# Performance work log

Hardware: AMD Instinct MI355X
Metric: run time of the kernel (lower is better)

The kernel has to match this reference:

```python
import jax, jax.numpy as jnp
import numpy as np

B, C, H, W = 4, 512, 64, 64
CQ = C // 8


def setup_inputs() -> dict:
    key = jax.random.key(0)
    k1, k2, k3, k4, k5 = jax.random.split(key, 5)
    return {
        "x": jax.random.normal(k1, (B, C, H, W), dtype=jnp.float32),
        "Wq": jax.random.normal(k2, (CQ, C), dtype=jnp.float32) * (2.0 / C) ** 0.5,
        "Wk": jax.random.normal(k3, (CQ, C), dtype=jnp.float32) * (2.0 / C) ** 0.5,
        "Wv": jax.random.normal(k4, (C, C), dtype=jnp.float32) * (2.0 / C) ** 0.5,
        "gamma": jax.random.normal(k5, (1,), dtype=jnp.float32),
    }


def reference(x, Wq, Wk, Wv, gamma):
    b, c, h, w = x.shape
    n = h * w
    xf = x.reshape(b, c, n)                       # (B, C, N)
    # 1x1 convs (bias=False, norm=identity) == channel matmuls
    q = jnp.einsum('qc,bcn->bnq', Wq, xf)         # (B, N, Cq) -- proj_query permuted
    k = jnp.einsum('qc,bcm->bqm', Wk, xf)         # (B, Cq, N) -- proj_key
    energy = jnp.einsum('bnq,bqm->bnm', q, k)     # (B, N, N)
    attn = jax.nn.softmax(energy, axis=-1)        # softmax over keys (last dim)
    v = jnp.einsum('dc,bcm->bdm', Wv, xf)         # (B, C, N) -- proj_value
    # out = bmm(V, attn^T): out[b,d,n] = sum_m V[b,d,m] * attn[b,n,m]
    out = jnp.einsum('bdm,bnm->bdn', v, attn).reshape(b, c, h, w)
    return gamma * out + x
```

## Files before the change

kernel.cpp:

```cpp
#include <hip/hip_runtime.h>

#define B_  4
#define C_  512
#define CQ_ 64
#define N_  4096
#define LOG2E 1.44269504088896f

typedef _Float16 half8 __attribute__((ext_vector_type(8)));
typedef _Float16 half4 __attribute__((ext_vector_type(4)));
typedef float    f32x4 __attribute__((ext_vector_type(4)));

__device__ __forceinline__ void g2l16(const void* g, void* l) {
  __builtin_amdgcn_global_load_lds(
      (const __attribute__((address_space(1))) void*)g,
      (__attribute__((address_space(3))) void*)l, 16, 0, 0);
}

__global__ __launch_bounds__(256) void wcvt_kernel(
    const float* __restrict__ Wq, const float* __restrict__ Wk,
    const float* __restrict__ Wv, _Float16* __restrict__ Wh)
{
  const int row = blockIdx.x;
  const float* src;
  float s = 1.0f;
  if (row < 64)       { src = Wq + (size_t)row * C_; s = LOG2E; }
  else if (row < 128) { src = Wk + (size_t)(row - 64) * C_; }
  else                { src = Wv + (size_t)(row - 128) * C_; }
  for (int c = threadIdx.x; c < C_; c += 256)
    Wh[(size_t)row * C_ + c] = (_Float16)(src[c] * s);
}

__global__ __launch_bounds__(256) void proj_kernel(
    const float* __restrict__ x, const _Float16* __restrict__ Wh,
    _Float16* __restrict__ Qh, _Float16* __restrict__ Kh, _Float16* __restrict__ Vh)
{
  __shared__ _Float16 xs[32][520];

  const int tid = threadIdx.x;
  const int wid = tid >> 6, lane = tid & 63, ln = lane & 15, lh = lane >> 4;

  const int wg = (blockIdx.x & 7) * 64 + (blockIdx.x >> 3);
  const int b  = wg >> 7;
  const int n0 = (wg & 127) * 32;

  {
    const int nn = (tid & 7) * 4;
    const int c0 = tid >> 3;
    #pragma unroll 4
    for (int cc = 0; cc < 16; ++cc) {
      const int c = cc * 32 + c0;
      f32x4 v = *(const f32x4*)&x[((size_t)b * C_ + c) * N_ + n0 + nn];
      #pragma unroll
      for (int u = 0; u < 4; ++u) xs[nn + u][c] = (_Float16)v[u];
    }
  }
  __syncthreads();

  for (int chT = 0; chT < 10; ++chT) {
    f32x4 acc[2] = {};
    const _Float16* wrow = Wh + (size_t)(chT * 64 + wid * 16 + ln) * C_;

    #pragma unroll 4
    for (int kt = 0; kt < C_; kt += 32) {
      half8 a = *(const half8*)&wrow[kt + lh * 8];
      #pragma unroll
      for (int ct = 0; ct < 2; ++ct) {
        half8 bf = *(const half8*)&xs[ct * 16 + ln][kt + lh * 8];
        acc[ct] = __builtin_amdgcn_mfma_f32_16x16x32_f16(a, bf, acc[ct], 0, 0, 0);
      }
    }

    #pragma unroll
    for (int ct = 0; ct < 2; ++ct) {
      const int n = n0 + ct * 16 + ln;
      #pragma unroll
      for (int j = 0; j < 4; ++j) {
        const int chL = wid * 16 + lh * 4 + j;
        const _Float16 v = (_Float16)acc[ct][j];
        if (chT == 0)      Qh[((size_t)b * N_ + n) * CQ_ + chL] = v;
        else if (chT == 1) Kh[((size_t)b * N_ + n) * CQ_ + chL] = v;
        else               Vh[((size_t)b * C_ + (chT - 2) * 64 + chL) * N_ + n] = v;
      }
    }
  }
}

__global__ __launch_bounds__(512, 2) void stats_kernel(
    const _Float16* __restrict__ Qh, const _Float16* __restrict__ Kh,
    float* __restrict__ m_g, float* __restrict__ il_g)
{
  __shared__ float Ms[8][64];
  __shared__ float Ss[8][64];

  const int tid = threadIdx.x;
  const int wid = tid >> 6, lane = tid & 63, ln = lane & 15, lh = lane >> 4;
  const int b  = blockIdx.x >> 6;
  const int qb = (blockIdx.x & 63) * 64;

  half8 qf[4][2];
  #pragma unroll
  for (int rt = 0; rt < 4; ++rt)
    #pragma unroll
    for (int h = 0; h < 2; ++h)
      qf[rt][h] = *(const half8*)&Qh[((size_t)b * N_ + qb + rt * 16 + ln) * CQ_ + h * 32 + lh * 8];

  float mx[4] = {-3.0e38f, -3.0e38f, -3.0e38f, -3.0e38f};
  float sm[4] = {0.f, 0.f, 0.f, 0.f};

  const _Float16* kp = Kh + ((size_t)b * N_ + wid * 16 + ln) * CQ_ + lh * 8;

  for (int it = 0; it < 32; ++it) {
    const _Float16* kq = kp + (size_t)(it * 128) * CQ_;
    half8 k0 = *(const half8*)kq;
    half8 k1 = *(const half8*)(kq + 32);
    #pragma unroll
    for (int rt = 0; rt < 4; ++rt) {
      f32x4 e = {};
      e = __builtin_amdgcn_mfma_f32_16x16x32_f16(k0, qf[rt][0], e, 0, 0, 0);
      e = __builtin_amdgcn_mfma_f32_16x16x32_f16(k1, qf[rt][1], e, 0, 0, 0);
      const float m1 = fmaxf(fmaxf(e[0], e[1]), fmaxf(e[2], e[3]));
      const float mn = fmaxf(mx[rt], m1);
      sm[rt] = sm[rt] * exp2f(mx[rt] - mn)
             + exp2f(e[0] - mn) + exp2f(e[1] - mn)
             + exp2f(e[2] - mn) + exp2f(e[3] - mn);
      mx[rt] = mn;
    }
  }

  #pragma unroll
  for (int rt = 0; rt < 4; ++rt) {
    float m = mx[rt], s = sm[rt];
    #pragma unroll
    for (int mask = 16; mask <= 32; mask <<= 1) {
      const float om = __shfl_xor(m, mask);
      const float os = __shfl_xor(s, mask);
      const float mn = fmaxf(m, om);
      s = s * exp2f(m - mn) + os * exp2f(om - mn);
      m = mn;
    }
    if (lane < 16) { Ms[wid][rt * 16 + lane] = m; Ss[wid][rt * 16 + lane] = s; }
  }
  __syncthreads();
  if (tid < 64) {
    float m = Ms[0][tid], s = Ss[0][tid];
    #pragma unroll
    for (int w = 1; w < 8; ++w) {
      const float om = Ms[w][tid], os = Ss[w][tid];
      const float mn = fmaxf(m, om);
      s = s * exp2f(m - mn) + os * exp2f(om - mn);
      m = mn;
    }
    m_g[(size_t)b * N_ + qb + tid]  = m;
    il_g[(size_t)b * N_ + qb + tid] = 1.0f / s;
  }
}

__global__ __launch_bounds__(256) void pwrite_kernel(
    const _Float16* __restrict__ Qh, const _Float16* __restrict__ Kh,
    const float* __restrict__ m_g, const float* __restrict__ il_g,
    _Float16* __restrict__ P, int b0)
{
  __shared__ _Float16 Pl[64 * 260];

  const int tid = threadIdx.x;
  const int wid = tid >> 6, lane = tid & 63, ln = lane & 15, lh = lane >> 4;
  const int mb = blockIdx.x * 256;
  const int qb = blockIdx.y * 64;
  const int bz = blockIdx.z;
  const int b  = b0 + bz;

  float m_l[4], il_l[4];
  #pragma unroll
  for (int rt = 0; rt < 4; ++rt) {
    m_l[rt]  = m_g [(size_t)b * N_ + qb + rt * 16 + ln];
    il_l[rt] = il_g[(size_t)b * N_ + qb + rt * 16 + ln];
  }

  half8 qf[4][2];
  #pragma unroll
  for (int rt = 0; rt < 4; ++rt)
    #pragma unroll
    for (int h = 0; h < 2; ++h)
      qf[rt][h] = *(const half8*)&Qh[((size_t)b * N_ + qb + rt * 16 + ln) * CQ_ + h * 32 + lh * 8];

  half8 kf[4][2];
  #pragma unroll
  for (int ms = 0; ms < 4; ++ms)
    #pragma unroll
    for (int h = 0; h < 2; ++h)
      kf[ms][h] = *(const half8*)&Kh[((size_t)b * N_ + mb + wid * 64 + ms * 16 + ln) * CQ_ + h * 32 + lh * 8];

  #pragma unroll
  for (int ms = 0; ms < 4; ++ms) {
    #pragma unroll
    for (int rt = 0; rt < 4; ++rt) {
      f32x4 e = {};
      e = __builtin_amdgcn_mfma_f32_16x16x32_f16(kf[ms][0], qf[rt][0], e, 0, 0, 0);
      e = __builtin_amdgcn_mfma_f32_16x16x32_f16(kf[ms][1], qf[rt][1], e, 0, 0, 0);
      half4 pv;
      #pragma unroll
      for (int j = 0; j < 4; ++j)
        pv[j] = (_Float16)(exp2f(e[j] - m_l[rt]) * il_l[rt]);
      *(half4*)&Pl[(rt * 16 + ln) * 260 + wid * 64 + ms * 16 + lh * 4] = pv;
    }
  }
  __syncthreads();

  const int row = tid >> 2;
  const int cb  = (tid & 3) * 8;
  #pragma unroll
  for (int i = 0; i < 8; ++i) {
    half8 v = *(const half8*)&Pl[row * 260 + cb + i * 32];
    *(half8*)&P[((size_t)bz * N_ + qb + row) * N_ + mb + cb + i * 32] = v;
  }
}

__global__ __launch_bounds__(512) void pv_kernel(
    const float* __restrict__ x, const _Float16* __restrict__ Vh,
    const _Float16* __restrict__ P, const float* __restrict__ gamma,
    float* __restrict__ out, int b0, int nwg)
{
  __shared__ _Float16 As[3][256 * 64];
  __shared__ _Float16 Bs[3][128 * 64];

  const int tid = threadIdx.x;
  const int wid = tid >> 6, lane = tid & 63, ln = lane & 15, lh = lane >> 4;

  const int q8 = nwg >> 3;
  const int wg = (blockIdx.x & 7) * q8 + (blockIdx.x >> 3);
  const int dt = wg & 1;
  const int nt = (wg >> 1) & 31;
  const int bz = wg >> 6;
  const int b  = b0 + bz;
  const int d0 = dt * 256, n0 = nt * 128;

  const _Float16* Ab = Vh + ((size_t)b * C_ + d0) * N_;
  const _Float16* Bb = P  + ((size_t)bz * N_ + n0) * N_;

  const int srow   = lane >> 3;
  const int schunk = lane & 7;
  const _Float16* aSrc[4];
  const _Float16* bSrc[2];
  #pragma unroll
  for (int r = 0; r < 4; ++r) {
    const int row = r * 64 + wid * 8 + srow;
    aSrc[r] = Ab + (size_t)row * N_ + ((schunk ^ (row & 7)) << 3);
  }
  #pragma unroll
  for (int r = 0; r < 2; ++r) {
    const int row = r * 64 + wid * 8 + srow;
    bSrc[r] = Bb + (size_t)row * N_ + ((schunk ^ (row & 7)) << 3);
  }

  auto stage = [&](int buf, int t) {
    const int m0 = t << 6;
    #pragma unroll
    for (int r = 0; r < 4; ++r)
      g2l16(aSrc[r] + m0, (char*)&As[buf][0] + r * 8192 + wid * 1024);
    #pragma unroll
    for (int r = 0; r < 2; ++r)
      g2l16(bSrc[r] + m0, (char*)&Bs[buf][0] + r * 8192 + wid * 1024);
  };

  const int wr = wid >> 1, wc = wid & 1;
  f32x4 acc[4][4] = {};
  const int swl = ln & 7;

  stage(0, 0);
  stage(1, 1);

  for (int t = 0; t < 64; ++t) {
    if (t < 63) { asm volatile("s_waitcnt vmcnt(6)" ::: "memory"); }
    else        { asm volatile("s_waitcnt vmcnt(0)" ::: "memory"); }
    __builtin_amdgcn_s_barrier();
    __builtin_amdgcn_sched_barrier(0);

    const int buf = t % 3;
    const _Float16* Ar = &As[buf][0];
    const _Float16* Br = &Bs[buf][0];

    half8 a[4][2], bq[4][2];
    #pragma unroll
    for (int ft = 0; ft < 4; ++ft) {
      const int row = wr * 64 + ft * 16 + ln;
      #pragma unroll
      for (int kk = 0; kk < 2; ++kk)
        a[ft][kk] = *(const half8*)&Ar[row * 64 + ((((kk << 2) | lh) ^ swl) << 3)];
    }
    #pragma unroll
    for (int gt = 0; gt < 4; ++gt) {
      const int row = wc * 64 + gt * 16 + ln;
      #pragma unroll
      for (int kk = 0; kk < 2; ++kk)
        bq[gt][kk] = *(const half8*)&Br[row * 64 + ((((kk << 2) | lh) ^ swl) << 3)];
    }

    if (t < 62) stage((t + 2) % 3, t + 2);

    #pragma unroll
    for (int kk = 0; kk < 2; ++kk)
      #pragma unroll
      for (int ft = 0; ft < 4; ++ft)
        #pragma unroll
        for (int gt = 0; gt < 4; ++gt)
          acc[ft][gt] = __builtin_amdgcn_mfma_f32_16x16x32_f16(a[ft][kk], bq[gt][kk], acc[ft][gt], 0, 0, 0);
  }

  const float g = gamma[0];
  #pragma unroll
  for (int ft = 0; ft < 4; ++ft) {
    #pragma unroll
    for (int gt = 0; gt < 4; ++gt) {
      #pragma unroll
      for (int j = 0; j < 4; ++j) {
        const int d = d0 + wr * 64 + ft * 16 + lh * 4 + j;
        const int n = n0 + wc * 64 + gt * 16 + ln;
        const size_t idx = ((size_t)b * C_ + d) * N_ + n;
        out[idx] = g * acc[ft][gt][j] + x[idx];
      }
    }
  }
}

extern "C" void kernel_launch(void* const* d_in, const int* in_sizes, int n_in,
                              void* d_out, int out_size, void* d_ws, size_t ws_size,
                              hipStream_t stream) {
  const float* x     = (const float*)d_in[0];
  const float* Wq    = (const float*)d_in[1];
  const float* Wk    = (const float*)d_in[2];
  const float* Wv    = (const float*)d_in[3];
  const float* gamma = (const float*)d_in[4];
  float* out = (float*)d_out;

  _Float16* Qh = (_Float16*)d_ws;
  _Float16* Kh = Qh + (size_t)B_ * N_ * CQ_;
  _Float16* Vh = Kh + (size_t)B_ * N_ * CQ_;
  float* m_g   = (float*)(Vh + (size_t)B_ * C_ * N_);
  float* il_g  = m_g + (size_t)B_ * N_;
  _Float16* Wh = (_Float16*)(il_g + (size_t)B_ * N_);
  _Float16* P  = Wh + (size_t)640 * C_;

  const size_t fixed = (size_t)((char*)P - (char*)d_ws);
  const int nb = (ws_size >= fixed + (size_t)B_ * N_ * N_ * sizeof(_Float16)) ? 4 : 2;

  wcvt_kernel<<<dim3(640), 256, 0, stream>>>(Wq, Wk, Wv, Wh);
  proj_kernel<<<dim3(512), 256, 0, stream>>>(x, Wh, Qh, Kh, Vh);
  stats_kernel<<<dim3(256), 512, 0, stream>>>(Qh, Kh, m_g, il_g);

  for (int b0 = 0; b0 < B_; b0 += nb) {
    pwrite_kernel<<<dim3(16, 64, nb), 256, 0, stream>>>(Qh, Kh, m_g, il_g, P, b0);
    pv_kernel<<<dim3(nb * 64), 512, 0, stream>>>(x, Vh, P, gamma, out, b0, nb * 64);
  }
}
```

Baseline: 190.0 us.

## Defer softmax normalization: max-only stats, row sums in pwrite, scale in epilogue

The stats kernel now computes only the row max, dropping the online exp-sum, which removes most of its exp2 work. The pwrite kernel stores unnormalized exp values and writes per-block partial row sums. A new small kernel reduces these sums into reciprocals, and pv_kernel applies the 1/sum scale together with gamma in its epilogue. The pv loop also issues the next stage's loads before the LDS fragment reads and raises wave priority around the MFMA block. The cost is an extra kernel launch per batch chunk and a partial-sum buffer, and storing unnormalized P in fp16 is safe only because every value is at most 1.

```diff
diff --git a/kernel.cpp b/kernel.cpp
--- a/kernel.cpp
+++ b/kernel.cpp
@@ -87,10 +87,9 @@
 
 __global__ __launch_bounds__(512, 2) void stats_kernel(
     const _Float16* __restrict__ Qh, const _Float16* __restrict__ Kh,
-    float* __restrict__ m_g, float* __restrict__ il_g)
+    float* __restrict__ m_g)
 {
   __shared__ float Ms[8][64];
-  __shared__ float Ss[8][64];
 
   const int tid = threadIdx.x;
   const int wid = tid >> 6, lane = tid & 63, ln = lane & 15, lh = lane >> 4;
@@ -105,7 +104,6 @@
       qf[rt][h] = *(const half8*)&Qh[((size_t)b * N_ + qb + rt * 16 + ln) * CQ_ + h * 32 + lh * 8];
 
   float mx[4] = {-3.0e38f, -3.0e38f, -3.0e38f, -3.0e38f};
-  float sm[4] = {0.f, 0.f, 0.f, 0.f};
 
   const _Float16* kp = Kh + ((size_t)b * N_ + wid * 16 + ln) * CQ_ + lh * 8;
 
@@ -118,49 +116,33 @@
       f32x4 e = {};
       e = __builtin_amdgcn_mfma_f32_16x16x32_f16(k0, qf[rt][0], e, 0, 0, 0);
       e = __builtin_amdgcn_mfma_f32_16x16x32_f16(k1, qf[rt][1], e, 0, 0, 0);
-      const float m1 = fmaxf(fmaxf(e[0], e[1]), fmaxf(e[2], e[3]));
-      const float mn = fmaxf(mx[rt], m1);
-      sm[rt] = sm[rt] * exp2f(mx[rt] - mn)
-             + exp2f(e[0] - mn) + exp2f(e[1] - mn)
-             + exp2f(e[2] - mn) + exp2f(e[3] - mn);
-      mx[rt] = mn;
+      mx[rt] = fmaxf(mx[rt], fmaxf(fmaxf(e[0], e[1]), fmaxf(e[2], e[3])));
     }
   }
 
   #pragma unroll
   for (int rt = 0; rt < 4; ++rt) {
-    float m = mx[rt], s = sm[rt];
-    #pragma unroll
-    for (int mask = 16; mask <= 32; mask <<= 1) {
-      const float om = __shfl_xor(m, mask);
-      const float os = __shfl_xor(s, mask);
-      const float mn = fmaxf(m, om);
-      s = s * exp2f(m - mn) + os * exp2f(om - mn);
-      m = mn;
-    }
-    if (lane < 16) { Ms[wid][rt * 16 + lane] = m; Ss[wid][rt * 16 + lane] = s; }
+    float m = mx[rt];
+    m = fmaxf(m, __shfl_xor(m, 16));
+    m = fmaxf(m, __shfl_xor(m, 32));
+    if (lane < 16) Ms[wid][rt * 16 + lane] = m;
   }
   __syncthreads();
   if (tid < 64) {
-    float m = Ms[0][tid], s = Ss[0][tid];
-    #pragma unroll
-    for (int w = 1; w < 8; ++w) {
-      const float om = Ms[w][tid], os = Ss[w][tid];
-      const float mn = fmaxf(m, om);
-      s = s * exp2f(m - mn) + os * exp2f(om - mn);
-      m = mn;
-    }
-    m_g[(size_t)b * N_ + qb + tid]  = m;
-    il_g[(size_t)b * N_ + qb + tid] = 1.0f / s;
+    float m = Ms[0][tid];
+    #pragma unroll
+    for (int w = 1; w < 8; ++w) m = fmaxf(m, Ms[w][tid]);
+    m_g[(size_t)b * N_ + qb + tid] = m;
   }
 }
 
 __global__ __launch_bounds__(256) void pwrite_kernel(
     const _Float16* __restrict__ Qh, const _Float16* __restrict__ Kh,
-    const float* __restrict__ m_g, const float* __restrict__ il_g,
+    const float* __restrict__ m_g, float* __restrict__ Lp,
     _Float16* __restrict__ P, int b0)
 {
   __shared__ _Float16 Pl[64 * 260];
+  __shared__ float    Ls[4][64];
 
   const int tid = threadIdx.x;
   const int wid = tid >> 6, lane = tid & 63, ln = lane & 15, lh = lane >> 4;
@@ -169,12 +151,10 @@
   const int bz = blockIdx.z;
   const int b  = b0 + bz;
 
-  float m_l[4], il_l[4];
-  #pragma unroll
-  for (int rt = 0; rt < 4; ++rt) {
-    m_l[rt]  = m_g [(size_t)b * N_ + qb + rt * 16 + ln];
-    il_l[rt] = il_g[(size_t)b * N_ + qb + rt * 16 + ln];
-  }
+  float m_l[4];
+  #pragma unroll
+  for (int rt = 0; rt < 4; ++rt)
+    m_l[rt] = m_g[(size_t)b * N_ + qb + rt * 16 + ln];
 
   half8 qf[4][2];
   #pragma unroll
@@ -189,6 +169,8 @@
     #pragma unroll
     for (int h = 0; h < 2; ++h)
       kf[ms][h] = *(const half8*)&Kh[((size_t)b * N_ + mb + wid * 64 + ms * 16 + ln) * CQ_ + h * 32 + lh * 8];
+
+  float psum[4] = {0.f, 0.f, 0.f, 0.f};
 
   #pragma unroll
   for (int ms = 0; ms < 4; ++ms) {
@@ -199,12 +181,27 @@
       e = __builtin_amdgcn_mfma_f32_16x16x32_f16(kf[ms][1], qf[rt][1], e, 0, 0, 0);
       half4 pv;
       #pragma unroll
-      for (int j = 0; j < 4; ++j)
-        pv[j] = (_Float16)(exp2f(e[j] - m_l[rt]) * il_l[rt]);
+      for (int j = 0; j < 4; ++j) {
+        const float p = exp2f(e[j] - m_l[rt]);
+        psum[rt] += p;
+        pv[j] = (_Float16)p;
+      }
       *(half4*)&Pl[(rt * 16 + ln) * 260 + wid * 64 + ms * 16 + lh * 4] = pv;
     }
   }
+
+  #pragma unroll
+  for (int rt = 0; rt < 4; ++rt) {
+    psum[rt] += __shfl_xor(psum[rt], 16);
+    psum[rt] += __shfl_xor(psum[rt], 32);
+    if (lane < 16) Ls[wid][rt * 16 + lane] = psum[rt];
+  }
   __syncthreads();
+
+  if (tid < 64) {
+    const float s = Ls[0][tid] + Ls[1][tid] + Ls[2][tid] + Ls[3][tid];
+    Lp[((size_t)blockIdx.x * B_ + b) * N_ + qb + tid] = s;
+  }
 
   const int row = tid >> 2;
   const int cb  = (tid & 3) * 8;
@@ -215,10 +212,23 @@
   }
 }
 
+__global__ __launch_bounds__(256) void lred_kernel(
+    const float* __restrict__ Lp, float* __restrict__ il_g, int b0)
+{
+  const int bz = blockIdx.x >> 4;
+  const int q  = (blockIdx.x & 15) * 256 + threadIdx.x;
+  const int b  = b0 + bz;
+  float s = 0.f;
+  #pragma unroll
+  for (int mb = 0; mb < 16; ++mb)
+    s += Lp[((size_t)mb * B_ + b) * N_ + q];
+  il_g[(size_t)b * N_ + q] = 1.0f / s;
+}
+
 __global__ __launch_bounds__(512) void pv_kernel(
     const float* __restrict__ x, const _Float16* __restrict__ Vh,
-    const _Float16* __restrict__ P, const float* __restrict__ gamma,
-    float* __restrict__ out, int b0, int nwg)
+    const _Float16* __restrict__ P, const float* __restrict__ il_g,
+    const float* __restrict__ gamma, float* __restrict__ out, int b0, int nwg)
 {
   __shared__ _Float16 As[3][256 * 64];
   __shared__ _Float16 Bs[3][128 * 64];
@@ -275,6 +285,8 @@
     __builtin_amdgcn_s_barrier();
     __builtin_amdgcn_sched_barrier(0);
 
+    if (t < 62) stage((t + 2) % 3, t + 2);
+
     const int buf = t % 3;
     const _Float16* Ar = &As[buf][0];
     const _Float16* Br = &Bs[buf][0];
@@ -295,8 +307,7 @@
         bq[gt][kk] = *(const half8*)&Br[row * 64 + ((((kk << 2) | lh) ^ swl) << 3)];
     }
 
-    if (t < 62) stage((t + 2) % 3, t + 2);
-
+    __builtin_amdgcn_s_setprio(1);
     #pragma unroll
     for (int kk = 0; kk < 2; ++kk)
       #pragma unroll
@@ -304,19 +315,26 @@
         #pragma unroll
         for (int gt = 0; gt < 4; ++gt)
           acc[ft][gt] = __builtin_amdgcn_mfma_f32_16x16x32_f16(a[ft][kk], bq[gt][kk], acc[ft][gt], 0, 0, 0);
+    __builtin_amdgcn_s_setprio(0);
   }
 
   const float g = gamma[0];
+  float il[4];
+  #pragma unroll
+  for (int gt = 0; gt < 4; ++gt)
+    il[gt] = il_g[(size_t)b * N_ + n0 + wc * 64 + gt * 16 + ln];
+
   #pragma unroll
   for (int ft = 0; ft < 4; ++ft) {
     #pragma unroll
     for (int gt = 0; gt < 4; ++gt) {
+      const float gi = g * il[gt];
       #pragma unroll
       for (int j = 0; j < 4; ++j) {
         const int d = d0 + wr * 64 + ft * 16 + lh * 4 + j;
         const int n = n0 + wc * 64 + gt * 16 + ln;
         const size_t idx = ((size_t)b * C_ + d) * N_ + n;
-        out[idx] = g * acc[ft][gt][j] + x[idx];
+        out[idx] = gi * acc[ft][gt][j] + x[idx];
       }
     }
   }
@@ -337,7 +355,8 @@
   _Float16* Vh = Kh + (size_t)B_ * N_ * CQ_;
   float* m_g   = (float*)(Vh + (size_t)B_ * C_ * N_);
   float* il_g  = m_g + (size_t)B_ * N_;
-  _Float16* Wh = (_Float16*)(il_g + (size_t)B_ * N_);
+  float* Lp    = il_g + (size_t)B_ * N_;
+  _Float16* Wh = (_Float16*)(Lp + (size_t)16 * B_ * N_);
   _Float16* P  = Wh + (size_t)640 * C_;
 
   const size_t fixed = (size_t)((char*)P - (char*)d_ws);
@@ -345,10 +364,11 @@
 
   wcvt_kernel<<<dim3(640), 256, 0, stream>>>(Wq, Wk, Wv, Wh);
   proj_kernel<<<dim3(512), 256, 0, stream>>>(x, Wh, Qh, Kh, Vh);
-  stats_kernel<<<dim3(256), 512, 0, stream>>>(Qh, Kh, m_g, il_g);
+  stats_kernel<<<dim3(256), 512, 0, stream>>>(Qh, Kh, m_g);
 
   for (int b0 = 0; b0 < B_; b0 += nb) {
-    pwrite_kernel<<<dim3(16, 64, nb), 256, 0, stream>>>(Qh, Kh, m_g, il_g, P, b0);
-    pv_kernel<<<dim3(nb * 64), 512, 0, stream>>>(x, Vh, P, gamma, out, b0, nb * 64);
-  }
-}
+    pwrite_kernel<<<dim3(16, 64, nb), 256, 0, stream>>>(Qh, Kh, m_g, Lp, P, b0);
+    lred_kernel<<<dim3(nb * 16), 256, 0, stream>>>(Lp, il_g, b0);
+    pv_kernel<<<dim3(nb * 64), 512, 0, stream>>>(x, Vh, P, il_g, gamma, out, b0, nb * 64);
+  }
+}
```

Result: slower. 249.9 us (+31.5%).
